# Kernel tuning notes

Measured on AMD Instinct MI355X. Metric: run time of the kernel, lower is better.

The kernel has to match this reference:

```python
import jax, jax.numpy as jnp
import numpy as np

EMB = 1024
HEAD = 64  # emb_size // head_nb = 1024 // 16

def setup_inputs() -> dict:
    key = jax.random.key(0)
    kx, kq, kk, kv = jax.random.split(key, 4)
    x = jax.random.normal(kx, (8, 2048, EMB), dtype=jnp.float32)
    # torch nn.Linear(EMB, HEAD) weight has shape [HEAD, EMB]; y = x @ W.T
    s = 1.0 / np.sqrt(EMB)
    Wq = jax.random.uniform(kq, (HEAD, EMB), jnp.float32, -s, s)
    Wk = jax.random.uniform(kk, (HEAD, EMB), jnp.float32, -s, s)
    Wv = jax.random.uniform(kv, (HEAD, EMB), jnp.float32, -s, s)
    return {"x": x, "Wq": Wq, "Wk": Wk, "Wv": Wv}

def reference(x, Wq, Wk, Wv):
    B, T, C = x.shape
    q = jnp.einsum('btc,hc->bth', x, Wq)  # [B,T,H]
    k = jnp.einsum('btc,hc->bth', x, Wk)
    v = jnp.einsum('btc,hc->bth', x, Wv)
    scale = 1.0 / jnp.sqrt(jnp.float32(q.shape[-1]))
    wei = jnp.einsum('bth,bsh->bts', q, k) * scale  # [B,T,T]
    causal = jnp.tril(jnp.ones((T, T), dtype=bool))
    wei = jnp.where(causal, wei, -jnp.inf)
    wei = jax.nn.softmax(wei, axis=-1)
    # dropout is identity in eval mode
    out = jnp.einsum('bts,bsh->bth', wei, v)  # [B,T,H]
    return out
```

## Files before the change

### kernel.cpp

```cpp
#include <hip/hip_runtime.h>
#include <math.h>

#define SEQ  2048
#define NROW 16384
#define HEAD 64
#define EMB  1024

typedef __attribute__((ext_vector_type(8))) short short8;
typedef __attribute__((ext_vector_type(4))) float f32x4;

static __device__ __forceinline__ unsigned short f2bf(float f) {
    unsigned u = __builtin_bit_cast(unsigned, f);
    u += 0x7fffu + ((u >> 16) & 1u);
    return (unsigned short)(u >> 16);
}
static __device__ __forceinline__ float bf2f(unsigned short u) {
    unsigned v = (unsigned)u << 16;
    return __builtin_bit_cast(float, v);
}
static __device__ __forceinline__ short8 cvt8(float4 a, float4 b) {
    short8 r;
    r[0] = f2bf(a.x); r[1] = f2bf(a.y); r[2] = f2bf(a.z); r[3] = f2bf(a.w);
    r[4] = f2bf(b.x); r[5] = f2bf(b.y); r[6] = f2bf(b.z); r[7] = f2bf(b.w);
    return r;
}
static __device__ __forceinline__ ushort4 cvt4(float4 f) {
    ushort4 u;
    u.x = f2bf(f.x); u.y = f2bf(f.y); u.z = f2bf(f.z); u.w = f2bf(f.w);
    return u;
}

static __device__ __forceinline__ void gload_lds16(const void* g, void* l) {
    __builtin_amdgcn_global_load_lds(
        (const __attribute__((address_space(1))) unsigned int*)g,
        (__attribute__((address_space(3))) unsigned int*)l, 16, 0, 0);
}

__global__ __launch_bounds__(256) void wcvt_kernel(
    const float* __restrict__ Wq, const float* __restrict__ Wk,
    const float* __restrict__ Wv, unsigned short* __restrict__ Wb)
{
    const int idx = (blockIdx.x * 256 + threadIdx.x) * 4;
    const int h = idx >> 10;
    const float* src;
    if (h < 64)       src = Wq + idx;
    else if (h < 128) src = Wk + (idx - 65536);
    else              src = Wv + (idx - 131072);
    *(ushort4*)(Wb + idx) = cvt4(*(const float4*)src);
}

__global__ __launch_bounds__(256, 3) void qkv_mfma_kernel(
    const float* __restrict__ x, const unsigned short* __restrict__ Wb,
    unsigned short* __restrict__ qN, unsigned short* __restrict__ kN,
    unsigned short* __restrict__ vT)
{
    __shared__ unsigned short As[2][64][72];
    __shared__ unsigned short Bs[2][96 * 64];

    const int tid  = threadIdx.x;
    const int w    = tid >> 6;
    const int lane = tid & 63;
    const int col  = lane & 15;
    const int quad = lane >> 4;
    const int row0 = blockIdx.x * 64;
    const int ny   = blockIdx.y;
    const int arow = w * 16 + col;
    const int pq   = (quad ^ (col & 7)) * 8;

    const int ar_r = tid >> 4, ar_c = tid & 15;
    const float* xg = x + (size_t)(row0 + ar_r) * EMB + ar_c * 4;

    const int sr = lane >> 3, cc = (lane & 7) ^ sr;
    const unsigned short* bg = Wb + (size_t)(ny * 96) * EMB;

    {
        float4 fa[4];
#pragma unroll
        for (int j = 0; j < 4; ++j) fa[j] = *(const float4*)(xg + (size_t)(16 * j) * EMB);
#pragma unroll
        for (int j = 0; j < 4; ++j) *(ushort4*)&As[0][ar_r + 16 * j][ar_c * 4] = cvt4(fa[j]);
#pragma unroll
        for (int j = 0; j < 3; ++j) {
            const int r = (w * 3 + j) * 8 + sr;
            gload_lds16(bg + (size_t)r * EMB + cc * 8, &Bs[0][(w * 3 + j) * 8 * 64]);
        }
    }
    __syncthreads();

    f32x4 acc[6];
#pragma unroll
    for (int t = 0; t < 6; ++t) acc[t] = (f32x4){0.f, 0.f, 0.f, 0.f};

    float4 fa[4];
#pragma unroll 2
    for (int kt = 0; kt < 16; ++kt) {
        const int cur = kt & 1;
        if (kt + 1 < 16) {
            const int k0 = (kt + 1) * 64;
#pragma unroll
            for (int j = 0; j < 3; ++j) {
                const int r = (w * 3 + j) * 8 + sr;
                gload_lds16(bg + (size_t)r * EMB + k0 + cc * 8,
                            &Bs[cur ^ 1][(w * 3 + j) * 8 * 64]);
            }
#pragma unroll
            for (int j = 0; j < 4; ++j)
                fa[j] = *(const float4*)(xg + (size_t)(16 * j) * EMB + k0);
        }
#pragma unroll
        for (int ks = 0; ks < 2; ++ks) {
            short8 af = *(const short8*)&As[cur][arow][ks * 32 + quad * 8];
            const int po = pq ^ (ks * 32);
#pragma unroll
            for (int t = 0; t < 6; ++t) {
                short8 bf = *(const short8*)&Bs[cur][(t * 16 + col) * 64 + po];
                acc[t] = __builtin_amdgcn_mfma_f32_16x16x32_bf16(af, bf, acc[t], 0, 0, 0);
            }
        }
        if (kt + 1 < 16) {
#pragma unroll
            for (int j = 0; j < 4; ++j)
                *(ushort4*)&As[cur ^ 1][ar_r + 16 * j][ar_c * 4] = cvt4(fa[j]);
        }
        __syncthreads();
    }

    const int ro = row0 + w * 16 + quad * 4;
#pragma unroll
    for (int t = 0; t < 6; ++t) {
        const int hb = ny * 96 + 16 * t;
        const int h  = hb + col;
        if (hb < 64) {
#pragma unroll
            for (int r = 0; r < 4; ++r)
                qN[(size_t)(ro + r) * HEAD + h] = f2bf(acc[t][r] * 0.125f);
        } else if (hb < 128) {
#pragma unroll
            for (int r = 0; r < 4; ++r)
                kN[(size_t)(ro + r) * HEAD + (h - 64)] = f2bf(acc[t][r]);
        } else {
            ushort4 uv;
            uv.x = f2bf(acc[t][0]); uv.y = f2bf(acc[t][1]);
            uv.z = f2bf(acc[t][2]); uv.w = f2bf(acc[t][3]);
            *(ushort4*)(vT + (size_t)(h - 128) * NROW + ro) = uv;
        }
    }
}

__global__ __launch_bounds__(256, 3) void attn_kernel(
    const unsigned short* __restrict__ qN,
    const unsigned short* __restrict__ kN,
    const unsigned short* __restrict__ vT,
    unsigned short* __restrict__ op,
    float2* __restrict__ ml)
{
    __shared__ unsigned short Ks[2][64 * 64];
    __shared__ unsigned short Vs[2][64 * 64];
    __shared__ float Pl[4][16][68];

    const int qt   = 31 - (int)blockIdx.x;
    const int b    = blockIdx.y;
    const int p    = blockIdx.z;
    const int tid  = threadIdx.x;
    const int wv   = tid >> 6;
    const int lane = tid & 63;
    const int col  = lane & 15;
    const int quad = lane >> 4;

    const int q0   = qt * 64 + wv * 16;
    const int q0g  = b * SEQ + q0;
    const int Cb   = qt + 1;
    const int kt0  = (Cb * p) >> 2;
    const int kt1  = (Cb * (p + 1)) >> 2;
    const int ktp  = min(kt0, Cb - 1);

    const int sr = lane >> 3, cc = (lane & 7) ^ sr;
    const int pq = (quad ^ (col & 7)) * 8;
    const unsigned short* kgb = kN + (size_t)(b * SEQ) * HEAD;
    const int bcol = b * SEQ;

    const short8* qp8 = (const short8*)qN + (size_t)(q0g + col) * 8;
    short8 aq0 = qp8[quad];
    short8 aq1 = qp8[quad + 4];

    f32x4 o[4];
#pragma unroll
    for (int t = 0; t < 4; ++t) o[t] = (f32x4){0.f, 0.f, 0.f, 0.f};
    float l_i[4] = {0.f, 0.f, 0.f, 0.f};

#pragma unroll
    for (int j = 0; j < 2; ++j) {
        const int r = (wv * 2 + j) * 8 + sr;
        gload_lds16(kgb + (size_t)(ktp * 64 + r) * HEAD + cc * 8,
                    &Ks[0][(wv * 2 + j) * 8 * 64]);
        gload_lds16(vT + (size_t)r * NROW + bcol + ktp * 64 + cc * 8,
                    &Vs[0][(wv * 2 + j) * 8 * 64]);
    }
    __syncthreads();

    for (int kt = kt0; kt < kt1; ++kt) {
        const int cur = (kt - kt0) & 1;
        const int s0  = kt * 64;
        const bool diag = (kt == Cb - 1);

        if (kt + 1 < kt1) {
#pragma unroll
            for (int j = 0; j < 2; ++j) {
                const int r = (wv * 2 + j) * 8 + sr;
                gload_lds16(kgb + (size_t)((kt + 1) * 64 + r) * HEAD + cc * 8,
                            &Ks[cur ^ 1][(wv * 2 + j) * 8 * 64]);
                gload_lds16(vT + (size_t)r * NROW + bcol + (kt + 1) * 64 + cc * 8,
                            &Vs[cur ^ 1][(wv * 2 + j) * 8 * 64]);
            }
        }

        f32x4 sv[4];
#pragma unroll
        for (int t = 0; t < 4; ++t) {
            const int rb = (16 * t + col) * 64;
            short8 kf0 = *(const short8*)&Ks[cur][rb + pq];
            short8 kf1 = *(const short8*)&Ks[cur][rb + (pq ^ 32)];
            sv[t] = (f32x4){0.f, 0.f, 0.f, 0.f};
            sv[t] = __builtin_amdgcn_mfma_f32_16x16x32_bf16(aq0, kf0, sv[t], 0, 0, 0);
            sv[t] = __builtin_amdgcn_mfma_f32_16x16x32_bf16(aq1, kf1, sv[t], 0, 0, 0);
        }

        float pv[4][4];
#pragma unroll
        for (int r = 0; r < 4; ++r) {
            const int grow = q0 + quad * 4 + r;
#pragma unroll
            for (int t = 0; t < 4; ++t) {
                float e = __expf(sv[t][r]);
                if (diag && (s0 + 16 * t + col > grow)) e = 0.0f;
                pv[t][r] = e;
            }
            l_i[r] += (pv[0][r] + pv[1][r]) + (pv[2][r] + pv[3][r]);
        }

#pragma unroll
        for (int t = 0; t < 4; ++t)
#pragma unroll
            for (int r = 0; r < 4; ++r)
                Pl[wv][quad * 4 + r][16 * t + col] = pv[t][r];
        short8 pf[2];
#pragma unroll
        for (int st = 0; st < 2; ++st) {
            float4 pa = *(const float4*)&Pl[wv][col][quad * 8 + 32 * st];
            float4 pb = *(const float4*)&Pl[wv][col][quad * 8 + 32 * st + 4];
            pf[st] = cvt8(pa, pb);
        }

#pragma unroll
        for (int tn = 0; tn < 4; ++tn) {
            const int rb = (16 * tn + col) * 64;
            short8 vf0 = *(const short8*)&Vs[cur][rb + pq];
            short8 vf1 = *(const short8*)&Vs[cur][rb + (pq ^ 32)];
            o[tn] = __builtin_amdgcn_mfma_f32_16x16x32_bf16(pf[0], vf0, o[tn], 0, 0, 0);
            o[tn] = __builtin_amdgcn_mfma_f32_16x16x32_bf16(pf[1], vf1, o[tn], 0, 0, 0);
        }

        __syncthreads();
    }

#pragma unroll
    for (int r = 0; r < 4; ++r) {
        float l = l_i[r];
        l += __shfl_xor(l, 1, 16);
        l += __shfl_xor(l, 2, 16);
        l += __shfl_xor(l, 4, 16);
        l += __shfl_xor(l, 8, 16);
        l_i[r] = l;
    }
#pragma unroll
    for (int tn = 0; tn < 4; ++tn)
#pragma unroll
        for (int r = 0; r < 4; ++r)
            op[((size_t)p * NROW + q0g + quad * 4 + r) * HEAD + 16 * tn + col] =
                f2bf(o[tn][r]);
    if (col == 0) {
#pragma unroll
        for (int r = 0; r < 4; ++r)
            ml[p * NROW + q0g + quad * 4 + r] = make_float2(0.0f, l_i[r]);
    }
}

__global__ __launch_bounds__(256) void merge_kernel(
    const unsigned short* __restrict__ op, const float2* __restrict__ ml,
    float* __restrict__ out)
{
    const int idx = blockIdx.x * 256 + threadIdx.x;
    const int row = idx >> 4;
    const int hc  = (idx & 15) * 4;

    float denom = 0.0f;
#pragma unroll
    for (int p = 0; p < 4; ++p) denom += ml[p * NROW + row].y;
    const float inv = 1.0f / denom;

    float4 r = make_float4(0.f, 0.f, 0.f, 0.f);
#pragma unroll
    for (int p = 0; p < 4; ++p) {
        ushort4 u = *(const ushort4*)(op + ((size_t)p * NROW + row) * HEAD + hc);
        r.x += bf2f(u.x);
        r.y += bf2f(u.y);
        r.z += bf2f(u.z);
        r.w += bf2f(u.w);
    }
    r.x *= inv; r.y *= inv; r.z *= inv; r.w *= inv;
    *(float4*)(out + (size_t)row * HEAD + hc) = r;
}

extern "C" void kernel_launch(void* const* d_in, const int* in_sizes, int n_in,
                              void* d_out, int out_size, void* d_ws, size_t ws_size,
                              hipStream_t stream)
{
    const float* x  = (const float*)d_in[0];
    const float* Wq = (const float*)d_in[1];
    const float* Wk = (const float*)d_in[2];
    const float* Wv = (const float*)d_in[3];

    char* w = (char*)d_ws;
    unsigned short* qN = (unsigned short*)w;
    unsigned short* kN = (unsigned short*)(w + (2u << 20));
    unsigned short* vT = (unsigned short*)(w + (4u << 20));
    unsigned short* Wb = (unsigned short*)(w + (6u << 20));
    unsigned short* op = (unsigned short*)(w + (6u << 20) + 393216);
    float2*         ml = (float2*)(w + (14u << 20) + 393216);
    float* out = (float*)d_out;

    wcvt_kernel<<<192, 256, 0, stream>>>(Wq, Wk, Wv, Wb);
    qkv_mfma_kernel<<<dim3(256, 2), 256, 0, stream>>>(x, Wb, qN, kN, vT);
    attn_kernel<<<dim3(32, 8, 4), 256, 0, stream>>>(qN, kN, vT, op, ml);
    merge_kernel<<<1024, 256, 0, stream>>>(op, ml, out);
}
```

Baseline: 140.4 us.

## Process two query sub-tiles per wave to reuse K/V tiles, store P as bf16

The attention kernel now covers 128 query rows per block, with each wave handling two 16-row sub-tiles, so every K/V tile loaded into LDS feeds twice as many MFMAs. The grid shrinks to half the query tiles. The diagonal masking is reworked so the upper sub-tile skips the last key tile. P is also converted to bf16 before going into LDS rather than stored as fp32, which halves the LDS traffic for that round trip. In exchange the kernel uses more registers per wave, which may lower occupancy, and it launches fewer blocks.

```diff
diff --git a/kernel.cpp b/kernel.cpp
--- a/kernel.cpp
+++ b/kernel.cpp
@@ -17,12 +17,6 @@
 static __device__ __forceinline__ float bf2f(unsigned short u) {
     unsigned v = (unsigned)u << 16;
     return __builtin_bit_cast(float, v);
-}
-static __device__ __forceinline__ short8 cvt8(float4 a, float4 b) {
-    short8 r;
-    r[0] = f2bf(a.x); r[1] = f2bf(a.y); r[2] = f2bf(a.z); r[3] = f2bf(a.w);
-    r[4] = f2bf(b.x); r[5] = f2bf(b.y); r[6] = f2bf(b.z); r[7] = f2bf(b.w);
-    return r;
 }
 static __device__ __forceinline__ ushort4 cvt4(float4 f) {
     ushort4 u;
@@ -156,9 +150,9 @@
 {
     __shared__ unsigned short Ks[2][64 * 64];
     __shared__ unsigned short Vs[2][64 * 64];
-    __shared__ float Pl[4][16][68];
-
-    const int qt   = 31 - (int)blockIdx.x;
+    __shared__ unsigned short Pl[4][32][72];
+
+    const int qt   = 15 - (int)blockIdx.x;
     const int b    = blockIdx.y;
     const int p    = blockIdx.z;
     const int tid  = threadIdx.x;
@@ -167,9 +161,9 @@
     const int col  = lane & 15;
     const int quad = lane >> 4;
 
-    const int q0   = qt * 64 + wv * 16;
+    const int q0   = qt * 128 + wv * 16;
     const int q0g  = b * SEQ + q0;
-    const int Cb   = qt + 1;
+    const int Cb   = 2 * qt + 2;
     const int kt0  = (Cb * p) >> 2;
     const int kt1  = (Cb * (p + 1)) >> 2;
     const int ktp  = min(kt0, Cb - 1);
@@ -179,14 +173,20 @@
     const unsigned short* kgb = kN + (size_t)(b * SEQ) * HEAD;
     const int bcol = b * SEQ;
 
-    const short8* qp8 = (const short8*)qN + (size_t)(q0g + col) * 8;
-    short8 aq0 = qp8[quad];
-    short8 aq1 = qp8[quad + 4];
-
-    f32x4 o[4];
-#pragma unroll
-    for (int t = 0; t < 4; ++t) o[t] = (f32x4){0.f, 0.f, 0.f, 0.f};
-    float l_i[4] = {0.f, 0.f, 0.f, 0.f};
+    const short8* qp0 = (const short8*)qN + (size_t)(q0g + col) * 8;
+    const short8* qp1 = (const short8*)qN + (size_t)(q0g + 64 + col) * 8;
+    short8 aq00 = qp0[quad], aq01 = qp0[quad + 4];
+    short8 aq10 = qp1[quad], aq11 = qp1[quad + 4];
+
+    f32x4 o[2][4];
+    float l_i[2][4];
+#pragma unroll
+    for (int mi = 0; mi < 2; ++mi)
+#pragma unroll
+        for (int t = 0; t < 4; ++t) {
+            o[mi][t] = (f32x4){0.f, 0.f, 0.f, 0.f};
+            l_i[mi][t] = 0.f;
+        }
 
 #pragma unroll
     for (int j = 0; j < 2; ++j) {
@@ -201,7 +201,8 @@
     for (int kt = kt0; kt < kt1; ++kt) {
         const int cur = (kt - kt0) & 1;
         const int s0  = kt * 64;
-        const bool diag = (kt == Cb - 1);
+        const bool dz = (kt >= Cb - 2);
+        const bool m0 = (kt < Cb - 1);
 
         if (kt + 1 < kt1) {
 #pragma unroll
@@ -214,74 +215,90 @@
             }
         }
 
-        f32x4 sv[4];
+        f32x4 sv[2][4];
+#pragma unroll
+        for (int t = 0; t < 4; ++t) {
+            sv[0][t] = (f32x4){0.f, 0.f, 0.f, 0.f};
+            sv[1][t] = (f32x4){0.f, 0.f, 0.f, 0.f};
+        }
 #pragma unroll
         for (int t = 0; t < 4; ++t) {
             const int rb = (16 * t + col) * 64;
             short8 kf0 = *(const short8*)&Ks[cur][rb + pq];
             short8 kf1 = *(const short8*)&Ks[cur][rb + (pq ^ 32)];
-            sv[t] = (f32x4){0.f, 0.f, 0.f, 0.f};
-            sv[t] = __builtin_amdgcn_mfma_f32_16x16x32_bf16(aq0, kf0, sv[t], 0, 0, 0);
-            sv[t] = __builtin_amdgcn_mfma_f32_16x16x32_bf16(aq1, kf1, sv[t], 0, 0, 0);
-        }
-
-        float pv[4][4];
-#pragma unroll
-        for (int r = 0; r < 4; ++r) {
-            const int grow = q0 + quad * 4 + r;
-#pragma unroll
-            for (int t = 0; t < 4; ++t) {
-                float e = __expf(sv[t][r]);
-                if (diag && (s0 + 16 * t + col > grow)) e = 0.0f;
-                pv[t][r] = e;
-            }
-            l_i[r] += (pv[0][r] + pv[1][r]) + (pv[2][r] + pv[3][r]);
-        }
-
-#pragma unroll
-        for (int t = 0; t < 4; ++t)
-#pragma unroll
-            for (int r = 0; r < 4; ++r)
-                Pl[wv][quad * 4 + r][16 * t + col] = pv[t][r];
-        short8 pf[2];
-#pragma unroll
-        for (int st = 0; st < 2; ++st) {
-            float4 pa = *(const float4*)&Pl[wv][col][quad * 8 + 32 * st];
-            float4 pb = *(const float4*)&Pl[wv][col][quad * 8 + 32 * st + 4];
-            pf[st] = cvt8(pa, pb);
-        }
+            sv[1][t] = __builtin_amdgcn_mfma_f32_16x16x32_bf16(aq10, kf0, sv[1][t], 0, 0, 0);
+            sv[1][t] = __builtin_amdgcn_mfma_f32_16x16x32_bf16(aq11, kf1, sv[1][t], 0, 0, 0);
+            if (m0) {
+                sv[0][t] = __builtin_amdgcn_mfma_f32_16x16x32_bf16(aq00, kf0, sv[0][t], 0, 0, 0);
+                sv[0][t] = __builtin_amdgcn_mfma_f32_16x16x32_bf16(aq01, kf1, sv[0][t], 0, 0, 0);
+            }
+        }
+
+#pragma unroll
+        for (int mi = 0; mi < 2; ++mi) {
+            if (mi == 0 && !m0) continue;
+#pragma unroll
+            for (int r = 0; r < 4; ++r) {
+                const int grow = q0 + mi * 64 + quad * 4 + r;
+                float ls = 0.f;
+#pragma unroll
+                for (int t = 0; t < 4; ++t) {
+                    float e = __expf(sv[mi][t][r]);
+                    if (dz && (s0 + 16 * t + col > grow)) e = 0.0f;
+                    Pl[wv][mi * 16 + quad * 4 + r][16 * t + col] = f2bf(e);
+                    ls += e;
+                }
+                l_i[mi][r] += ls;
+            }
+        }
+
+        short8 pf00, pf01;
+        if (m0) {
+            pf00 = *(const short8*)&Pl[wv][col][quad * 8];
+            pf01 = *(const short8*)&Pl[wv][col][quad * 8 + 32];
+        }
+        short8 pf10 = *(const short8*)&Pl[wv][16 + col][quad * 8];
+        short8 pf11 = *(const short8*)&Pl[wv][16 + col][quad * 8 + 32];
 
 #pragma unroll
         for (int tn = 0; tn < 4; ++tn) {
             const int rb = (16 * tn + col) * 64;
             short8 vf0 = *(const short8*)&Vs[cur][rb + pq];
             short8 vf1 = *(const short8*)&Vs[cur][rb + (pq ^ 32)];
-            o[tn] = __builtin_amdgcn_mfma_f32_16x16x32_bf16(pf[0], vf0, o[tn], 0, 0, 0);
-            o[tn] = __builtin_amdgcn_mfma_f32_16x16x32_bf16(pf[1], vf1, o[tn], 0, 0, 0);
+            o[1][tn] = __builtin_amdgcn_mfma_f32_16x16x32_bf16(pf10, vf0, o[1][tn], 0, 0, 0);
+            o[1][tn] = __builtin_amdgcn_mfma_f32_16x16x32_bf16(pf11, vf1, o[1][tn], 0, 0, 0);
+            if (m0) {
+                o[0][tn] = __builtin_amdgcn_mfma_f32_16x16x32_bf16(pf00, vf0, o[0][tn], 0, 0, 0);
+                o[0][tn] = __builtin_amdgcn_mfma_f32_16x16x32_bf16(pf01, vf1, o[0][tn], 0, 0, 0);
+            }
         }
 
         __syncthreads();
     }
 
 #pragma unroll
-    for (int r = 0; r < 4; ++r) {
-        float l = l_i[r];
-        l += __shfl_xor(l, 1, 16);
-        l += __shfl_xor(l, 2, 16);
-        l += __shfl_xor(l, 4, 16);
-        l += __shfl_xor(l, 8, 16);
-        l_i[r] = l;
-    }
-#pragma unroll
-    for (int tn = 0; tn < 4; ++tn)
-#pragma unroll
-        for (int r = 0; r < 4; ++r)
-            op[((size_t)p * NROW + q0g + quad * 4 + r) * HEAD + 16 * tn + col] =
-                f2bf(o[tn][r]);
-    if (col == 0) {
-#pragma unroll
-        for (int r = 0; r < 4; ++r)
-            ml[p * NROW + q0g + quad * 4 + r] = make_float2(0.0f, l_i[r]);
+    for (int mi = 0; mi < 2; ++mi) {
+#pragma unroll
+        for (int r = 0; r < 4; ++r) {
+            float l = l_i[mi][r];
+            l += __shfl_xor(l, 1, 16);
+            l += __shfl_xor(l, 2, 16);
+            l += __shfl_xor(l, 4, 16);
+            l += __shfl_xor(l, 8, 16);
+            l_i[mi][r] = l;
+        }
+        const int ro = q0g + mi * 64 + quad * 4;
+#pragma unroll
+        for (int tn = 0; tn < 4; ++tn)
+#pragma unroll
+            for (int r = 0; r < 4; ++r)
+                op[((size_t)p * NROW + ro + r) * HEAD + 16 * tn + col] =
+                    f2bf(o[mi][tn][r]);
+        if (col == 0) {
+#pragma unroll
+            for (int r = 0; r < 4; ++r)
+                ml[p * NROW + ro + r] = make_float2(0.0f, l_i[mi][r]);
+        }
     }
 }
 
@@ -331,6 +348,6 @@
 
     wcvt_kernel<<<192, 256, 0, stream>>>(Wq, Wk, Wv, Wb);
     qkv_mfma_kernel<<<dim3(256, 2), 256, 0, stream>>>(x, Wb, qN, kN, vT);
-    attn_kernel<<<dim3(32, 8, 4), 256, 0, stream>>>(qN, kN, vT, op, ml);
+    attn_kernel<<<dim3(16, 8, 4), 256, 0, stream>>>(qN, kN, vT, op, ml);
     merge_kernel<<<1024, 256, 0, stream>>>(op, ml, out);
 }
```

Result: no change. 138.2 us (-1.6%).
